# Performance work log

Measured on AMD Instinct MI355X. Metric: run time of the kernel, lower is better.

The kernel has to match this reference:

```python
import jax, jax.numpy as jnp
import numpy as np

N_NODES = 1_000_000
N_GRAPHS = 20_000
C, M, N_GEN = 10, 50, 8


def setup_inputs() -> dict:
    key = jax.random.key(0)
    k1, k2, k3, k4 = jax.random.split(key, 4)
    x = jax.random.randint(k1, (N_NODES,), 0, M, dtype=jnp.int64 if jax.config.jax_enable_x64 else jnp.int32)
    batch = jnp.sort(jax.random.randint(k2, (N_NODES,), 0, N_GRAPHS, dtype=jnp.int64 if jax.config.jax_enable_x64 else jnp.int32))
    B = jax.random.normal(k3, (C, M, N_GEN), dtype=jnp.float32) * 2.0
    Pi = jax.random.normal(k4, (C, N_GEN), dtype=jnp.float32) * 2.0
    return {"x": x, "batch": batch, "B": B, "Pi": Pi}


def reference(x, batch, B, Pi):
    # softmax reparameterization: per-generator softmax over M (for B) and over C (for Pi)
    sm_B = jax.nn.softmax(B, axis=1)            # [C, M, n_gen]
    sm_Pi = jax.nn.softmax(Pi, axis=0)          # [C, n_gen]

    # gather emission probs for each node's label: sm_B[:, x] -> [C, N, n_gen] -> [N, C, n_gen]
    emit = jnp.transpose(jnp.take(sm_B, x, axis=1), (1, 0, 2))  # [N, C, n_gen]
    numerator = sm_Pi[None, :, :] * emit                        # [N, C, n_gen]

    posterior = numerator / jnp.sum(numerator, axis=1, keepdims=True)
    likelihood = jnp.sum(posterior * jnp.log(numerator), axis=1)  # [N, n_gen]

    # scatter-sum per graph
    likelihood = jax.ops.segment_sum(likelihood, batch, num_segments=N_GRAPHS)  # [G, n_gen]

    h_states = jnp.argmax(posterior, axis=1)  # [N, n_gen]
    return likelihood, h_states
```

## Files before the change

### kernel.cpp

```cpp
#include <hip/hip_runtime.h>

#define NN 1000000
#define NG 20000
#define C_ 10
#define M_ 50
#define G_ 8

__global__ __launch_bounds__(256) void k_fused(const float* __restrict__ B,
                                               const float* __restrict__ Pi,
                                               const int* __restrict__ x,
                                               const int* __restrict__ batch,
                                               float* __restrict__ out,
                                               float* __restrict__ outh) {
    __shared__ float sB[C_ * M_ * G_];
    __shared__ float sPi[C_ * G_];
    __shared__ float sZB[C_ * G_];
    __shared__ float sZP[G_];
    __shared__ float lik[M_ * 9];
    __shared__ float hst[M_ * 9];
    __shared__ int   sx[1024];
    __shared__ int   sb[1025];
    __shared__ int   heads[1024];
    __shared__ int   hcnt;
    __shared__ int   s_is64;

    const int t = threadIdx.x;
    const int base = blockIdx.x * 1024;
    const int limit = (NN - base < 1024) ? (NN - base) : 1024;

    if (t < 64) {
        const int v = x[2 * t + 1] | x[128 + 2 * t + 1];
        const unsigned long long nz = __ballot(v != 0);
        if (t == 0) { s_is64 = (nz == 0ULL) ? 1 : 0; hcnt = 0; }
    } else if (t < 144) {
        sPi[t - 64] = Pi[t - 64];
    }
    for (int i = t; i < C_ * M_ * G_ / 4; i += 256)
        ((float4*)sB)[i] = ((const float4*)B)[i];
    __syncthreads();
    const int is64 = s_is64;

    if (t < 80) {
        const int c = t >> 3, g = t & 7;
        float Z = 0.f;
        for (int m = 0; m < M_; ++m) Z += __expf(sB[(c * M_ + m) * G_ + g]);
        sZB[t] = __logf(Z);
    } else if (t < 88) {
        const int g = t - 80;
        float Z = 0.f;
        for (int c = 0; c < C_; ++c) Z += __expf(sPi[c * G_ + g]);
        sZP[g] = __logf(Z);
    } else if (t >= 128) {
        if (is64) {
            const int4* xq = (const int4*)x + (base >> 1);
            const int4* bq = (const int4*)batch + (base >> 1);
            for (int i = t - 128; i < (limit >> 1); i += 128) {
                const int4 v = xq[i];
                sx[2 * i] = v.x; sx[2 * i + 1] = v.z;
                const int4 w = bq[i];
                sb[1 + 2 * i] = w.x; sb[2 + 2 * i] = w.z;
            }
            if (t == 128) sb[0] = (base == 0) ? -1 : batch[2 * (base - 1)];
        } else {
            const int4* xq = (const int4*)x + (base >> 2);
            const int4* bq = (const int4*)batch + (base >> 2);
            for (int i = t - 128; i < (limit >> 2); i += 128) {
                const int4 v = xq[i];
                sx[4 * i] = v.x; sx[4 * i + 1] = v.y; sx[4 * i + 2] = v.z; sx[4 * i + 3] = v.w;
                const int4 w = bq[i];
                sb[1 + 4 * i] = w.x; sb[2 + 4 * i] = w.y; sb[3 + 4 * i] = w.z; sb[4 + 4 * i] = w.w;
            }
            if (t == 128) sb[0] = (base == 0) ? -1 : batch[base - 1];
        }
    }
    __syncthreads();

    for (int e = t; e < M_ * G_; e += 256) {
        const int m = e >> 3, g = e & 7;
        float s[C_];
        float bv = -1e30f;
        int bi = 0;
        for (int c = 0; c < C_; ++c) {
            const float v = (sB[(c * M_ + m) * G_ + g] - sZB[c * G_ + g]) +
                            (sPi[c * G_ + g] - sZP[g]);
            s[c] = v;
            if (v > bv) { bv = v; bi = c; }
        }
        float Z = 0.f, W = 0.f;
        for (int c = 0; c < C_; ++c) {
            const float ee = __expf(s[c]);
            Z += ee;
            W += ee * s[c];
        }
        lik[m * 9 + g] = W / Z;
        hst[m * 9 + g] = (float)bi;
    }
    if (4 * t < limit) {
#pragma unroll
        for (int k = 0; k < 4; ++k) {
            const int i = 4 * t + k;
            if (sb[1 + i] != sb[i])
                heads[atomicAdd(&hcnt, 1)] = i;
        }
    }
    __syncthreads();

    float4* op = (float4*)outh + (size_t)base * 2;
    const int nf4 = limit * 2;
    for (int idx = t; idx < nf4; idx += 256) {
        const int xi = sx[idx >> 1];
        const int o = xi * 9 + (idx & 1) * 4;
        float4 v;
        v.x = hst[o]; v.y = hst[o + 1]; v.z = hst[o + 2]; v.w = hst[o + 3];
        op[idx] = v;
    }

    const int wid = t >> 6, lane = t & 63;
    const int ns = lane >> 3, r = lane & 7;
    const int H = hcnt;
    for (int j = wid; j < H; j += 4) {
        const int i0 = heads[j];
        const int g  = sb[1 + i0];
        const int gp = sb[i0];
        if (lane < 8)
            for (int gg = gp + 1; gg < g; ++gg)
                out[(size_t)gg * 8 + lane] = 0.f;

        const int n0 = base + i0;
        int n_end = NN;
        for (int bse = n0; ; bse += 64) {
            const int ii = bse + lane;
            int val = g + 1;
            if (ii < NN)
                val = (ii < base + limit) ? sb[1 + ii - base]
                                          : (is64 ? batch[2 * (size_t)ii] : batch[ii]);
            const unsigned long long diff = __ballot(val != g);
            if (diff) { n_end = bse + (int)__builtin_ctzll(diff); break; }
        }

        float acc = 0.f;
        for (int n = n0 + ns; n < n_end; n += 8) {
            const int xi = (n < base + limit) ? sx[n - base]
                                              : (is64 ? x[2 * (size_t)n] : x[n]);
            acc += lik[xi * 9 + r];
        }
        acc += __shfl_xor(acc, 8, 64);
        acc += __shfl_xor(acc, 16, 64);
        acc += __shfl_xor(acc, 32, 64);
        if (lane < 8) out[(size_t)g * 8 + lane] = acc;

        if (n_end == NN && lane < 8)
            for (int gg = g + 1; gg < NG; ++gg)
                out[(size_t)gg * 8 + lane] = 0.f;
    }
}

extern "C" void kernel_launch(void* const* d_in, const int* in_sizes, int n_in,
                              void* d_out, int out_size, void* d_ws, size_t ws_size,
                              hipStream_t stream) {
    const int*   x     = (const int*)d_in[0];
    const int*   batch = (const int*)d_in[1];
    const float* B     = (const float*)d_in[2];
    const float* Pi    = (const float*)d_in[3];
    float* out  = (float*)d_out;
    float* outh = (float*)d_out + NG * G_;

    k_fused<<<(NN + 1023) / 1024, 256, 0, stream>>>(B, Pi, x, batch, out, outh);
}
```

Baseline: 24.10 us.

## Read B and Pi directly from global, drop staging sync, vectorize hstate table

Removes the shared-memory staging of the 16KB B table and Pi, along with the first __syncthreads, and instead reads B/Pi straight from global memory (L1/L2 cached) in the normalizer and posterior loops. Every wave now runs its own is64 detection via ballot, so the node/batch loads use all 256 threads instead of 128. The hidden-state table is stored in a split float4 layout, so the output loop does one vector LDS read per float4 store instead of four scalar reads. The cost is uncoalesced, strided global reads of B in the per-(m,g) loops and redundant detection loads in each wave.

```diff
diff --git a/kernel.cpp b/kernel.cpp
--- a/kernel.cpp
+++ b/kernel.cpp
@@ -12,66 +12,57 @@
                                                const int* __restrict__ batch,
                                                float* __restrict__ out,
                                                float* __restrict__ outh) {
-    __shared__ float sB[C_ * M_ * G_];
-    __shared__ float sPi[C_ * G_];
     __shared__ float sZB[C_ * G_];
     __shared__ float sZP[G_];
     __shared__ float lik[M_ * 9];
-    __shared__ float hst[M_ * 9];
+    __shared__ float hstf[2 * M_ * 4];
     __shared__ int   sx[1024];
     __shared__ int   sb[1025];
     __shared__ int   heads[1024];
     __shared__ int   hcnt;
-    __shared__ int   s_is64;
 
     const int t = threadIdx.x;
+    const int lane = t & 63;
     const int base = blockIdx.x * 1024;
     const int limit = (NN - base < 1024) ? (NN - base) : 1024;
 
-    if (t < 64) {
-        const int v = x[2 * t + 1] | x[128 + 2 * t + 1];
-        const unsigned long long nz = __ballot(v != 0);
-        if (t == 0) { s_is64 = (nz == 0ULL) ? 1 : 0; hcnt = 0; }
-    } else if (t < 144) {
-        sPi[t - 64] = Pi[t - 64];
+    if (t == 0) hcnt = 0;
+
+    const int vdet = x[2 * lane + 1] | x[128 + 2 * lane + 1];
+    const int is64 = (__ballot(vdet != 0) == 0ULL) ? 1 : 0;
+
+    if (is64) {
+        const int4* xq = (const int4*)x + (base >> 1);
+        const int4* bq = (const int4*)batch + (base >> 1);
+        for (int i = t; i < (limit >> 1); i += 256) {
+            const int4 a = xq[i];
+            sx[2 * i] = a.x; sx[2 * i + 1] = a.z;
+            const int4 w = bq[i];
+            sb[1 + 2 * i] = w.x; sb[2 + 2 * i] = w.z;
+        }
+        if (t == 0) sb[0] = (base == 0) ? -1 : batch[2 * (base - 1)];
+    } else {
+        const int4* xq = (const int4*)x + (base >> 2);
+        const int4* bq = (const int4*)batch + (base >> 2);
+        for (int i = t; i < (limit >> 2); i += 256) {
+            const int4 a = xq[i];
+            sx[4 * i] = a.x; sx[4 * i + 1] = a.y; sx[4 * i + 2] = a.z; sx[4 * i + 3] = a.w;
+            const int4 w = bq[i];
+            sb[1 + 4 * i] = w.x; sb[2 + 4 * i] = w.y; sb[3 + 4 * i] = w.z; sb[4 + 4 * i] = w.w;
+        }
+        if (t == 0) sb[0] = (base == 0) ? -1 : batch[base - 1];
     }
-    for (int i = t; i < C_ * M_ * G_ / 4; i += 256)
-        ((float4*)sB)[i] = ((const float4*)B)[i];
-    __syncthreads();
-    const int is64 = s_is64;
 
     if (t < 80) {
         const int c = t >> 3, g = t & 7;
         float Z = 0.f;
-        for (int m = 0; m < M_; ++m) Z += __expf(sB[(c * M_ + m) * G_ + g]);
+        for (int m = 0; m < M_; ++m) Z += __expf(B[(c * M_ + m) * G_ + g]);
         sZB[t] = __logf(Z);
     } else if (t < 88) {
         const int g = t - 80;
         float Z = 0.f;
-        for (int c = 0; c < C_; ++c) Z += __expf(sPi[c * G_ + g]);
+        for (int c = 0; c < C_; ++c) Z += __expf(Pi[c * G_ + g]);
         sZP[g] = __logf(Z);
-    } else if (t >= 128) {
-        if (is64) {
-            const int4* xq = (const int4*)x + (base >> 1);
-            const int4* bq = (const int4*)batch + (base >> 1);
-            for (int i = t - 128; i < (limit >> 1); i += 128) {
-                const int4 v = xq[i];
-                sx[2 * i] = v.x; sx[2 * i + 1] = v.z;
-                const int4 w = bq[i];
-                sb[1 + 2 * i] = w.x; sb[2 + 2 * i] = w.z;
-            }
-            if (t == 128) sb[0] = (base == 0) ? -1 : batch[2 * (base - 1)];
-        } else {
-            const int4* xq = (const int4*)x + (base >> 2);
-            const int4* bq = (const int4*)batch + (base >> 2);
-            for (int i = t - 128; i < (limit >> 2); i += 128) {
-                const int4 v = xq[i];
-                sx[4 * i] = v.x; sx[4 * i + 1] = v.y; sx[4 * i + 2] = v.z; sx[4 * i + 3] = v.w;
-                const int4 w = bq[i];
-                sb[1 + 4 * i] = w.x; sb[2 + 4 * i] = w.y; sb[3 + 4 * i] = w.z; sb[4 + 4 * i] = w.w;
-            }
-            if (t == 128) sb[0] = (base == 0) ? -1 : batch[base - 1];
-        }
     }
     __syncthreads();
 
@@ -81,8 +72,8 @@
         float bv = -1e30f;
         int bi = 0;
         for (int c = 0; c < C_; ++c) {
-            const float v = (sB[(c * M_ + m) * G_ + g] - sZB[c * G_ + g]) +
-                            (sPi[c * G_ + g] - sZP[g]);
+            const float v = (B[(c * M_ + m) * G_ + g] - sZB[c * G_ + g]) +
+                            (Pi[c * G_ + g] - sZP[g]);
             s[c] = v;
             if (v > bv) { bv = v; bi = c; }
         }
@@ -93,7 +84,7 @@
             W += ee * s[c];
         }
         lik[m * 9 + g] = W / Z;
-        hst[m * 9 + g] = (float)bi;
+        hstf[((g >> 2) * M_ + m) * 4 + (g & 3)] = (float)bi;
     }
     if (4 * t < limit) {
 #pragma unroll
@@ -106,16 +97,14 @@
     __syncthreads();
 
     float4* op = (float4*)outh + (size_t)base * 2;
+    const float4* h4 = (const float4*)hstf;
     const int nf4 = limit * 2;
     for (int idx = t; idx < nf4; idx += 256) {
         const int xi = sx[idx >> 1];
-        const int o = xi * 9 + (idx & 1) * 4;
-        float4 v;
-        v.x = hst[o]; v.y = hst[o + 1]; v.z = hst[o + 2]; v.w = hst[o + 3];
-        op[idx] = v;
+        op[idx] = h4[(idx & 1) * M_ + xi];
     }
 
-    const int wid = t >> 6, lane = t & 63;
+    const int wid = t >> 6;
     const int ns = lane >> 3, r = lane & 7;
     const int H = hcnt;
     for (int j = wid; j < H; j += 4) {
```

Result: no change. 24.40 us (+1.3%).
